# Performance work log

Hardware: AMD Instinct MI355X
Metric: run time of the kernel (lower is better)

The kernel has to match this reference:

```python
import jax, jax.numpy as jnp
import numpy as np

B, S, D = 4, 2048, 1024
H = 16
HD = D // H  # 64


def setup_inputs() -> dict:
    key = jax.random.key(0)
    k0, k1, k2, k3, k4 = jax.random.split(key, 5)
    scale = 1.0 / np.sqrt(D)
    return {
        "x": jax.random.normal(k0, (B, S, D), dtype=jnp.float32),
        "Wq": jax.random.normal(k1, (D, D), dtype=jnp.float32) * scale,
        "Wk": jax.random.normal(k2, (D, D), dtype=jnp.float32) * scale,
        "Wv": jax.random.normal(k3, (D, D), dtype=jnp.float32) * scale,
        "Wo": jax.random.normal(k4, (D, D), dtype=jnp.float32) * scale,
    }


def reference(x, Wq, Wk, Wv, Wo):
    # nn.Linear(bias=False): y = x @ W.T, W is [out, in]
    def proj(W):
        y = jnp.einsum('bsd,ed->bse', x, W)          # [B,S,D]
        return y.reshape(B, S, H, HD).transpose(0, 2, 1, 3)  # [B,H,S,HD]

    q, k, v = proj(Wq), proj(Wk), proj(Wv)
    scores = jnp.einsum('bhqd,bhkd->bhqk', q, k) / np.sqrt(HD)  # [B,H,S,S]
    attn = jax.nn.softmax(scores, axis=-1)
    out = jnp.einsum('bhqk,bhkd->bhqd', attn, v)     # [B,H,S,HD]
    out = out.transpose(0, 2, 1, 3).reshape(B, S, D)  # [B,S,D]
    return jnp.einsum('bsd,ed->bse', out, Wo)
```

## Files before the change

kernel.cpp:

```cpp
#include <hip/hip_runtime.h>
#include <hip/hip_bf16.h>
#include <cstdint>
#include <cstddef>

#define DEV __device__ __forceinline__

typedef __attribute__((ext_vector_type(8))) __bf16 bfrag8;
typedef __attribute__((ext_vector_type(4))) float f32x4;
typedef __attribute__((ext_vector_type(8))) unsigned short u16x8;
typedef __attribute__((ext_vector_type(4))) unsigned short u16x4;

static constexpr int S = 2048, D = 1024;
static constexpr size_t XN = (size_t)4 * 2048 * 1024;
static constexpr size_t WN = (size_t)1024 * 1024;

DEV unsigned short bfu(float f) {
  return __builtin_bit_cast(unsigned short, (__bf16)f);
}

#define GLOAD16(g, l)                                                          \
  __builtin_amdgcn_global_load_lds(                                            \
      (const __attribute__((address_space(1))) void*)(g),                      \
      (__attribute__((address_space(3))) void*)(l), 16, 0, 0)

__global__ __launch_bounds__(256) void convert_kernel(
    const float* __restrict__ x, const float* __restrict__ wq,
    const float* __restrict__ wk, const float* __restrict__ wv,
    const float* __restrict__ wo, unsigned short* __restrict__ dst) {
  size_t i = ((size_t)blockIdx.x * 256 + threadIdx.x) * 8;
  const float* src;
  size_t off;
  if (i < XN) { src = x; off = i; }
  else if (i < XN + WN)     { src = wq; off = i - XN; }
  else if (i < XN + 2 * WN) { src = wk; off = i - (XN + WN); }
  else if (i < XN + 3 * WN) { src = wv; off = i - (XN + 2 * WN); }
  else                      { src = wo; off = i - (XN + 3 * WN); }
  const float4* p = (const float4*)(src + off);
  float4 a = p[0], b = p[1];
  u16x8 o;
  o[0] = bfu(a.x); o[1] = bfu(a.y); o[2] = bfu(a.z); o[3] = bfu(a.w);
  o[4] = bfu(b.x); o[5] = bfu(b.y); o[6] = bfu(b.z); o[7] = bfu(b.w);
  *(u16x8*)(dst + i) = o;
}

DEV void gemm_mainloop(const unsigned short* __restrict__ Ag,
                       const unsigned short* __restrict__ Bg,
                       unsigned short* ldsA, unsigned short* ldsB,
                       f32x4 (&acc)[4][4], int tid) {
  const int lane = tid & 63;
  const int wr = (tid >> 7) & 1;
  const int wc = (tid >> 6) & 1;
  for (int kt = 0; kt < 32; ++kt) {
#pragma unroll
    for (int i = 0; i < 2; ++i) {
      const int c = tid + i * 256;
      const int row = c >> 2, ks = c & 3;
      const int ldsoff = ((tid & ~63) + i * 256) * 16;
      GLOAD16(Ag + (size_t)row * 1024 + kt * 32 + ks * 8, (char*)ldsA + ldsoff);
      GLOAD16(Bg + (size_t)row * 1024 + kt * 32 + ks * 8, (char*)ldsB + ldsoff);
    }
    asm volatile("s_waitcnt vmcnt(0)" ::: "memory");
    __syncthreads();
    bfrag8 av[4], bv[4];
#pragma unroll
    for (int m = 0; m < 4; ++m)
      av[m] = *(const bfrag8*)(ldsA + (wr * 64 + m * 16 + (lane & 15)) * 32 +
                               (lane >> 4) * 8);
#pragma unroll
    for (int n = 0; n < 4; ++n)
      bv[n] = *(const bfrag8*)(ldsB + (wc * 64 + n * 16 + (lane & 15)) * 32 +
                               (lane >> 4) * 8);
#pragma unroll
    for (int m = 0; m < 4; ++m)
#pragma unroll
      for (int n = 0; n < 4; ++n)
        acc[m][n] =
            __builtin_amdgcn_mfma_f32_16x16x32_bf16(av[m], bv[n], acc[m][n], 0, 0, 0);
    __syncthreads();
  }
}

__global__ __launch_bounds__(256, 2) void gemm_qkv(
    const unsigned short* __restrict__ xbf, const unsigned short* __restrict__ wq,
    const unsigned short* __restrict__ wk, const unsigned short* __restrict__ wv,
    unsigned short* __restrict__ Qb, unsigned short* __restrict__ Kb,
    unsigned short* __restrict__ Vt) {
  __shared__ __align__(16) unsigned short ldsA[128 * 32];
  __shared__ __align__(16) unsigned short ldsB[128 * 32];
  const int tid = threadIdx.x;
  const int z = blockIdx.z;
  const unsigned short* W = (z == 0) ? wq : ((z == 1) ? wk : wv);
  const int m0 = blockIdx.y * 128, n0 = blockIdx.x * 128;

  f32x4 acc[4][4];
#pragma unroll
  for (int m = 0; m < 4; ++m)
#pragma unroll
    for (int n = 0; n < 4; ++n) acc[m][n] = (f32x4){0.f, 0.f, 0.f, 0.f};

  gemm_mainloop(xbf + (size_t)m0 * 1024, W + (size_t)n0 * 1024, ldsA, ldsB, acc, tid);

  const int lane = tid & 63;
  const int wr = (tid >> 7) & 1, wc = (tid >> 6) & 1;
  const int hi = lane >> 4, lo = lane & 15;
  if (z < 2) {
    unsigned short* dst = (z == 0) ? Qb : Kb;
#pragma unroll
    for (int m = 0; m < 4; ++m)
#pragma unroll
      for (int n = 0; n < 4; ++n)
#pragma unroll
        for (int r = 0; r < 4; ++r) {
          int row = m0 + wr * 64 + m * 16 + hi * 4 + r;
          int col = n0 + wc * 64 + n * 16 + lo;
          dst[(size_t)row * 1024 + col] = bfu(acc[m][n][r]);
        }
  } else {
#pragma unroll
    for (int m = 0; m < 4; ++m)
#pragma unroll
      for (int n = 0; n < 4; ++n) {
        int col = n0 + wc * 64 + n * 16 + lo;
        int hh = col >> 6, hd = col & 63;
        int row0 = m0 + wr * 64 + m * 16 + hi * 4;
        int b_ = row0 >> 11, s_ = row0 & 2047;
        u16x4 pk;
#pragma unroll
        for (int r = 0; r < 4; ++r) pk[r] = bfu(acc[m][n][r]);
        *(u16x4*)(Vt + ((size_t)((b_ * 16 + hh) * 64 + hd)) * 2048 + s_) = pk;
      }
  }
}

__global__ __launch_bounds__(256, 2) void gemm_out(
    const unsigned short* __restrict__ Ob, const unsigned short* __restrict__ wo,
    float* __restrict__ out) {
  __shared__ __align__(16) unsigned short ldsA[128 * 32];
  __shared__ __align__(16) unsigned short ldsB[128 * 32];
  const int tid = threadIdx.x;
  const int m0 = blockIdx.y * 128, n0 = blockIdx.x * 128;
  f32x4 acc[4][4];
#pragma unroll
  for (int m = 0; m < 4; ++m)
#pragma unroll
    for (int n = 0; n < 4; ++n) acc[m][n] = (f32x4){0.f, 0.f, 0.f, 0.f};
  gemm_mainloop(Ob + (size_t)m0 * 1024, wo + (size_t)n0 * 1024, ldsA, ldsB, acc, tid);
  const int lane = tid & 63;
  const int wr = (tid >> 7) & 1, wc = (tid >> 6) & 1;
  const int hi = lane >> 4, lo = lane & 15;
#pragma unroll
  for (int m = 0; m < 4; ++m)
#pragma unroll
    for (int n = 0; n < 4; ++n)
#pragma unroll
      for (int r = 0; r < 4; ++r) {
        int row = m0 + wr * 64 + m * 16 + hi * 4 + r;
        int col = n0 + wc * 64 + n * 16 + lo;
        out[(size_t)row * 1024 + col] = acc[m][n][r];
      }
}

__global__ __launch_bounds__(256, 2) void attn_kernel(
    const unsigned short* __restrict__ Qb, const unsigned short* __restrict__ Kb,
    const unsigned short* __restrict__ Vt, unsigned short* __restrict__ Ob) {
  __shared__ __align__(16) unsigned short Plds[128 * 64];
  __shared__ __align__(16) unsigned short Klds[64 * 64];
  __shared__ __align__(16) unsigned short Vlds[64 * 64];

  const int tid = threadIdx.x, lane = tid & 63, wave = tid >> 6;
  const int hi = lane >> 4, lo = lane & 15;
  const int bh = blockIdx.y, b = bh >> 4, h = bh & 15;
  const int qt = blockIdx.x;

  const unsigned short* Qg = Qb + (size_t)(b * S + qt * 128) * D + h * 64;
  const unsigned short* Kg = Kb + (size_t)b * S * D + h * 64;
  const unsigned short* Vg = Vt + (size_t)bh * 64 * S;

  bfrag8 qf[2][2];
#pragma unroll
  for (int m = 0; m < 2; ++m)
#pragma unroll
    for (int kk = 0; kk < 2; ++kk)
      qf[m][kk] =
          *(const bfrag8*)(Qg + (size_t)(wave * 32 + m * 16 + lo) * D + kk * 32 + hi * 8);

  f32x4 oA[2][4];
  float mrow[2][4], lrow[2][4];
#pragma unroll
  for (int m = 0; m < 2; ++m) {
#pragma unroll
    for (int n = 0; n < 4; ++n) oA[m][n] = (f32x4){0.f, 0.f, 0.f, 0.f};
#pragma unroll
    for (int r = 0; r < 4; ++r) { mrow[m][r] = -INFINITY; lrow[m][r] = 0.f; }
  }
  const float c1 = 0.125f * 1.4426950408889634f;

  for (int kv0 = 0; kv0 < S; kv0 += 64) {
#pragma unroll
    for (int i = 0; i < 2; ++i) {
      int c = tid + i * 256;
      int row = c >> 3, sl = (c & 7) ^ (row & 7);
      int ldsoff = ((tid & ~63) + i * 256) * 16;
      GLOAD16(Kg + (size_t)(kv0 + row) * D + sl * 8, (char*)Klds + ldsoff);
      GLOAD16(Vg + (size_t)row * S + kv0 + sl * 8, (char*)Vlds + ldsoff);
    }
    asm volatile("s_waitcnt vmcnt(0)" ::: "memory");
    __syncthreads();

    bfrag8 kf[4][2];
#pragma unroll
    for (int n = 0; n < 4; ++n)
#pragma unroll
      for (int kk = 0; kk < 2; ++kk) {
        int row = n * 16 + lo;
        int slot = (kk * 4 + hi) ^ (row & 7);
        kf[n][kk] = *(const bfrag8*)(Klds + row * 64 + slot * 8);
      }
    f32x4 sc[2][4];
#pragma unroll
    for (int m = 0; m < 2; ++m)
#pragma unroll
      for (int n = 0; n < 4; ++n) {
        sc[m][n] = (f32x4){0.f, 0.f, 0.f, 0.f};
#pragma unroll
        for (int kk = 0; kk < 2; ++kk)
          sc[m][n] = __builtin_amdgcn_mfma_f32_16x16x32_bf16(qf[m][kk], kf[n][kk],
                                                             sc[m][n], 0, 0, 0);
      }

#pragma unroll
    for (int m = 0; m < 2; ++m)
#pragma unroll
      for (int r = 0; r < 4; ++r) {
        float mx = fmaxf(fmaxf(sc[m][0][r], sc[m][1][r]),
                         fmaxf(sc[m][2][r], sc[m][3][r]));
        mx = fmaxf(mx, __shfl_xor(mx, 1));
        mx = fmaxf(mx, __shfl_xor(mx, 2));
        mx = fmaxf(mx, __shfl_xor(mx, 4));
        mx = fmaxf(mx, __shfl_xor(mx, 8));
        float Mnew = fmaxf(mrow[m][r], mx * c1);
        float alpha = __builtin_amdgcn_exp2f(mrow[m][r] - Mnew);
        float psum = 0.f;
#pragma unroll
        for (int n = 0; n < 4; ++n) {
          float p = __builtin_amdgcn_exp2f(sc[m][n][r] * c1 - Mnew);
          sc[m][n][r] = p;
          psum += p;
        }
        psum += __shfl_xor(psum, 1);
        psum += __shfl_xor(psum, 2);
        psum += __shfl_xor(psum, 4);
        psum += __shfl_xor(psum, 8);
        lrow[m][r] = lrow[m][r] * alpha + psum;
        mrow[m][r] = Mnew;
#pragma unroll
        for (int n = 0; n < 4; ++n) oA[m][n][r] *= alpha;
      }

#pragma unroll
    for (int m = 0; m < 2; ++m)
#pragma unroll
      for (int n = 0; n < 4; ++n)
#pragma unroll
        for (int r = 0; r < 4; ++r) {
          int q = wave * 32 + m * 16 + hi * 4 + r;
          int kv = n * 16 + lo;
          int sl = (kv >> 3) ^ (q & 7);
          Plds[q * 64 + sl * 8 + (kv & 7)] = bfu(sc[m][n][r]);
        }

    bfrag8 pf[2][2], vf[4][2];
#pragma unroll
    for (int m = 0; m < 2; ++m)
#pragma unroll
      for (int kk = 0; kk < 2; ++kk) {
        int row = wave * 32 + m * 16 + lo;
        int slot = (kk * 4 + hi) ^ (row & 7);
        pf[m][kk] = *(const bfrag8*)(Plds + row * 64 + slot * 8);
      }
#pragma unroll
    for (int n = 0; n < 4; ++n)
#pragma unroll
      for (int kk = 0; kk < 2; ++kk) {
        int row = n * 16 + lo;
        int slot = (kk * 4 + hi) ^ (row & 7);
        vf[n][kk] = *(const bfrag8*)(Vlds + row * 64 + slot * 8);
      }
#pragma unroll
    for (int m = 0; m < 2; ++m)
#pragma unroll
      for (int n = 0; n < 4; ++n)
#pragma unroll
        for (int kk = 0; kk < 2; ++kk)
          oA[m][n] = __builtin_amdgcn_mfma_f32_16x16x32_bf16(pf[m][kk], vf[n][kk],
                                                             oA[m][n], 0, 0, 0);
    __syncthreads();
  }

#pragma unroll
  for (int m = 0; m < 2; ++m)
#pragma unroll
    for (int r = 0; r < 4; ++r) {
      float inv = 1.f / lrow[m][r];
      int q = wave * 32 + m * 16 + hi * 4 + r;
      size_t rowbase = (size_t)(b * S + qt * 128 + q) * D + h * 64;
#pragma unroll
      for (int n = 0; n < 4; ++n)
        Ob[rowbase + n * 16 + lo] = bfu(oA[m][n][r] * inv);
    }
}

extern "C" void kernel_launch(void* const* d_in, const int* in_sizes, int n_in,
                              void* d_out, int out_size, void* d_ws, size_t ws_size,
                              hipStream_t stream) {
  const float* x = (const float*)d_in[0];
  const float* wq = (const float*)d_in[1];
  const float* wk = (const float*)d_in[2];
  const float* wv = (const float*)d_in[3];
  const float* wo = (const float*)d_in[4];
  float* out = (float*)d_out;

  unsigned short* base = (unsigned short*)d_ws;
  unsigned short* xbf = base;
  unsigned short* wqb = xbf + XN;
  unsigned short* wkb = wqb + WN;
  unsigned short* wvb = wkb + WN;
  unsigned short* wob = wvb + WN;
  unsigned short* Qb = wob + WN;
  unsigned short* Kb = Qb + XN;
  unsigned short* Vt = Kb + XN;
  unsigned short* Ob = Vt + XN;

  convert_kernel<<<dim3(6144), dim3(256), 0, stream>>>(x, wq, wk, wv, wo, xbf);
  gemm_qkv<<<dim3(8, 64, 3), dim3(256), 0, stream>>>(xbf, wqb, wkb, wvb, Qb, Kb, Vt);
  attn_kernel<<<dim3(16, 64), dim3(256), 0, stream>>>(Qb, Kb, Vt, Ob);
  gemm_out<<<dim3(8, 64), dim3(256), 0, stream>>>(Ob, wob, out);
}
```

Before: 399.5 us.

## Double-buffer K/V tiles in attention and shrink per-wave P staging

The attention kernel now prefetches the next K/V tile into a second LDS buffer while computing on the current one, so global load latency overlaps with the MFMA and softmax work. The P scratch shrinks to a per-wave 16-row buffer that is reused for each m sub-tile, which cuts LDS use so the launch bound can ask for 4 blocks per CU. The grid is flattened to 1D with a remap of block index to (bh, qt) that spreads neighbouring blocks across heads, and s_setprio is raised around the MFMA sections. The costs are more LDS for the double buffer and more register pressure under the tighter occupancy target.

```diff
diff --git a/kernel.cpp b/kernel.cpp
--- a/kernel.cpp
+++ b/kernel.cpp
@@ -160,21 +160,25 @@
       }
 }
 
-__global__ __launch_bounds__(256, 2) void attn_kernel(
+__global__ __launch_bounds__(256, 4) void attn_kernel(
     const unsigned short* __restrict__ Qb, const unsigned short* __restrict__ Kb,
     const unsigned short* __restrict__ Vt, unsigned short* __restrict__ Ob) {
-  __shared__ __align__(16) unsigned short Plds[128 * 64];
-  __shared__ __align__(16) unsigned short Klds[64 * 64];
-  __shared__ __align__(16) unsigned short Vlds[64 * 64];
+  __shared__ __align__(16) unsigned short Plds[4 * 16 * 64];
+  __shared__ __align__(16) unsigned short Klds[2][64 * 64];
+  __shared__ __align__(16) unsigned short Vlds[2][64 * 64];
 
   const int tid = threadIdx.x, lane = tid & 63, wave = tid >> 6;
   const int hi = lane >> 4, lo = lane & 15;
-  const int bh = blockIdx.y, b = bh >> 4, h = bh & 15;
-  const int qt = blockIdx.x;
+
+  const int lin = blockIdx.x;
+  const int wid = (lin & 7) * 128 + (lin >> 3);
+  const int bh = wid >> 4, qt = wid & 15;
+  const int b = bh >> 4, h = bh & 15;
 
   const unsigned short* Qg = Qb + (size_t)(b * S + qt * 128) * D + h * 64;
   const unsigned short* Kg = Kb + (size_t)b * S * D + h * 64;
   const unsigned short* Vg = Vt + (size_t)bh * 64 * S;
+  unsigned short* Pw = Plds + wave * 16 * 64;
 
   bfrag8 qf[2][2];
 #pragma unroll
@@ -195,17 +199,27 @@
   }
   const float c1 = 0.125f * 1.4426950408889634f;
 
-  for (int kv0 = 0; kv0 < S; kv0 += 64) {
+  auto stage = [&](int buf, int kv0) {
 #pragma unroll
     for (int i = 0; i < 2; ++i) {
       int c = tid + i * 256;
       int row = c >> 3, sl = (c & 7) ^ (row & 7);
       int ldsoff = ((tid & ~63) + i * 256) * 16;
-      GLOAD16(Kg + (size_t)(kv0 + row) * D + sl * 8, (char*)Klds + ldsoff);
-      GLOAD16(Vg + (size_t)row * S + kv0 + sl * 8, (char*)Vlds + ldsoff);
+      GLOAD16(Kg + (size_t)(kv0 + row) * D + sl * 8, (char*)&Klds[buf][0] + ldsoff);
+      GLOAD16(Vg + (size_t)row * S + kv0 + sl * 8, (char*)&Vlds[buf][0] + ldsoff);
     }
-    asm volatile("s_waitcnt vmcnt(0)" ::: "memory");
-    __syncthreads();
+  };
+
+  stage(0, 0);
+  asm volatile("s_waitcnt vmcnt(0)" ::: "memory");
+  __syncthreads();
+  int cur = 0;
+
+  for (int t = 0; t < 32; ++t) {
+    if (t < 31) stage(cur ^ 1, (t + 1) * 64);
+
+    const unsigned short* Kc = &Klds[cur][0];
+    const unsigned short* Vc = &Vlds[cur][0];
 
     bfrag8 kf[4][2];
 #pragma unroll
@@ -214,9 +228,10 @@
       for (int kk = 0; kk < 2; ++kk) {
         int row = n * 16 + lo;
         int slot = (kk * 4 + hi) ^ (row & 7);
-        kf[n][kk] = *(const bfrag8*)(Klds + row * 64 + slot * 8);
+        kf[n][kk] = *(const bfrag8*)(Kc + row * 64 + slot * 8);
       }
     f32x4 sc[2][4];
+    __builtin_amdgcn_s_setprio(1);
 #pragma unroll
     for (int m = 0; m < 2; ++m)
 #pragma unroll
@@ -227,6 +242,7 @@
           sc[m][n] = __builtin_amdgcn_mfma_f32_16x16x32_bf16(qf[m][kk], kf[n][kk],
                                                              sc[m][n], 0, 0, 0);
       }
+    __builtin_amdgcn_s_setprio(0);
 
 #pragma unroll
     for (int m = 0; m < 2; ++m)
@@ -257,44 +273,46 @@
         for (int n = 0; n < 4; ++n) oA[m][n][r] *= alpha;
       }
 
-#pragma unroll
-    for (int m = 0; m < 2; ++m)
-#pragma unroll
-      for (int n = 0; n < 4; ++n)
-#pragma unroll
-        for (int r = 0; r < 4; ++r) {
-          int q = wave * 32 + m * 16 + hi * 4 + r;
-          int kv = n * 16 + lo;
-          int sl = (kv >> 3) ^ (q & 7);
-          Plds[q * 64 + sl * 8 + (kv & 7)] = bfu(sc[m][n][r]);
-        }
-
-    bfrag8 pf[2][2], vf[4][2];
-#pragma unroll
-    for (int m = 0; m < 2; ++m)
-#pragma unroll
-      for (int kk = 0; kk < 2; ++kk) {
-        int row = wave * 32 + m * 16 + lo;
-        int slot = (kk * 4 + hi) ^ (row & 7);
-        pf[m][kk] = *(const bfrag8*)(Plds + row * 64 + slot * 8);
-      }
+    bfrag8 vf[4][2];
 #pragma unroll
     for (int n = 0; n < 4; ++n)
 #pragma unroll
       for (int kk = 0; kk < 2; ++kk) {
         int row = n * 16 + lo;
         int slot = (kk * 4 + hi) ^ (row & 7);
-        vf[n][kk] = *(const bfrag8*)(Vlds + row * 64 + slot * 8);
-      }
-#pragma unroll
-    for (int m = 0; m < 2; ++m)
+        vf[n][kk] = *(const bfrag8*)(Vc + row * 64 + slot * 8);
+      }
+
+#pragma unroll
+    for (int m = 0; m < 2; ++m) {
+#pragma unroll
+      for (int n = 0; n < 4; ++n)
+#pragma unroll
+        for (int r = 0; r < 4; ++r) {
+          int q = hi * 4 + r;
+          int kv = n * 16 + lo;
+          int sl = (kv >> 3) ^ (q & 7);
+          Pw[q * 64 + sl * 8 + (kv & 7)] = bfu(sc[m][n][r]);
+        }
+      bfrag8 pf[2];
+#pragma unroll
+      for (int kk = 0; kk < 2; ++kk) {
+        int slot = (kk * 4 + hi) ^ (lo & 7);
+        pf[kk] = *(const bfrag8*)(Pw + lo * 64 + slot * 8);
+      }
+      __builtin_amdgcn_s_setprio(1);
 #pragma unroll
       for (int n = 0; n < 4; ++n)
 #pragma unroll
         for (int kk = 0; kk < 2; ++kk)
-          oA[m][n] = __builtin_amdgcn_mfma_f32_16x16x32_bf16(pf[m][kk], vf[n][kk],
+          oA[m][n] = __builtin_amdgcn_mfma_f32_16x16x32_bf16(pf[kk], vf[n][kk],
                                                              oA[m][n], 0, 0, 0);
+      __builtin_amdgcn_s_setprio(0);
+    }
+
+    asm volatile("s_waitcnt vmcnt(0)" ::: "memory");
     __syncthreads();
+    cur ^= 1;
   }
 
 #pragma unroll
@@ -333,6 +351,6 @@
 
   convert_kernel<<<dim3(6144), dim3(256), 0, stream>>>(x, wq, wk, wv, wo, xbf);
   gemm_qkv<<<dim3(8, 64, 3), dim3(256), 0, stream>>>(xbf, wqb, wkb, wvb, Qb, Kb, Vt);
-  attn_kernel<<<dim3(16, 64), dim3(256), 0, stream>>>(Qb, Kb, Vt, Ob);
+  attn_kernel<<<dim3(1024), dim3(256), 0, stream>>>(Qb, Kb, Vt, Ob);
   gemm_out<<<dim3(8, 64), dim3(256), 0, stream>>>(Ob, wob, out);
 }
```

Result: slower. 458.3 us (+14.7%).
